# Kernel tuning notes

Hardware: AMD Instinct MI355X
Metric: run time of the kernel (lower is better)

The kernel has to match this reference:

```python
import jax, jax.numpy as jnp
import numpy as np

N_NODES = 100000
N_EDGES = 1600000
NODE_F = 64
EDGE_F = 16
OUT_F = 64


def setup_inputs() -> dict:
    key = jax.random.key(0)
    k1, k2, k3, k4, k5 = jax.random.split(key, 5)
    feat = jax.random.normal(k1, (N_NODES, NODE_F), dtype=jnp.float32)
    edge_feats = jax.random.normal(k2, (N_EDGES, EDGE_F), dtype=jnp.float32)
    src = jax.random.randint(k3, (N_EDGES,), 0, N_NODES, dtype=jnp.int64)
    dst = jax.random.randint(k4, (N_EDGES,), 0, N_NODES, dtype=jnp.int64)
    # xavier-normal-ish weight, zero bias (matches reset_parameters)
    fan_in, fan_out = NODE_F + EDGE_F, OUT_F
    std = (2.0 / (fan_in + fan_out)) ** 0.5
    weight = jax.random.normal(k5, (fan_in, fan_out), dtype=jnp.float32) * std
    bias = jnp.zeros((OUT_F,), dtype=jnp.float32)
    return {"feat": feat, "edge_feats": edge_feats, "src": src, "dst": dst,
            "weight": weight, "bias": bias}


def reference(feat, edge_feats, src, dst, weight, bias):
    N = feat.shape[0]
    # in-degree based symmetric-ish norm: pow(clamp(in_deg,1), -0.5)
    deg = jax.ops.segment_sum(jnp.ones(dst.shape, dtype=feat.dtype), dst,
                              num_segments=N)
    norm = jnp.clip(deg, 1.0) ** -0.5  # [N]
    norm = norm[:, None]
    # sum over incoming edges of concat([edge_feats, h_src]).
    # sum of concat == concat of sums, so aggregate each part separately
    # (avoids materializing the per-edge concat).
    sum_e = jax.ops.segment_sum(edge_feats, dst, num_segments=N)  # [N, E_F]
    sum_h = jax.ops.segment_sum(feat[src], dst, num_segments=N)   # [N, NODE_F]
    sum_f = jnp.concatenate([sum_e, sum_h], axis=-1)              # [N, E_F+NODE_F]
    out = (sum_f * norm) @ weight
    out = out * norm + bias
    return jax.nn.selu(out)
```

## Files before the change

kernel.cpp:

```cpp
#include <hip/hip_runtime.h>
#include <math.h>

#define N_NODES 100000
#define N_EDGES 1600000
#define OUT_F   64
#define NCHUNK  98

#define EQ4      (N_EDGES / 4)
#define CNT_BLK  ((EQ4 + 255) / 256)
#define GEMM_BLK 512
#define K_E      18

typedef __attribute__((ext_vector_type(8))) short bf16x8;
typedef __attribute__((ext_vector_type(4))) float f32x4;

__device__ __forceinline__ unsigned short f2bf_rne(float f) {
    unsigned u = __float_as_uint(f);
    return (unsigned short)((u + 0x7fffu + ((u >> 16) & 1u)) >> 16);
}
__device__ __forceinline__ float bf2f(unsigned short h) {
    return __uint_as_float((unsigned)h << 16);
}

__global__ __launch_bounds__(256) void count_gemm(
    const int* __restrict__ dst, unsigned* __restrict__ pcnt,
    const float* __restrict__ feat, const float* __restrict__ weight,
    unsigned short* __restrict__ G)
{
    __shared__ unsigned lbin[NCHUNK];
    int tid = threadIdx.x;

    if (blockIdx.x < CNT_BLK) {
        if (tid < NCHUNK) lbin[tid] = 0u;
        __syncthreads();
        int q = blockIdx.x * 256 + tid;
        if (q < EQ4) {
            int4 d = ((const int4*)dst)[q];
            atomicAdd(&lbin[d.x >> 10], 1u);
            atomicAdd(&lbin[d.y >> 10], 1u);
            atomicAdd(&lbin[d.z >> 10], 1u);
            atomicAdd(&lbin[d.w >> 10], 1u);
        }
        __syncthreads();
        if (tid < NCHUNK)
            pcnt[(size_t)blockIdx.x * NCHUNK + tid] = lbin[tid];
        return;
    }

    int gb = (int)blockIdx.x - CNT_BLK;
    int wv = tid >> 6, ln = tid & 63;
    int li = ln & 15, lk = ln >> 4;

    bf16x8 Whi[4][2], Wlo[4][2];
    #pragma unroll
    for (int it = 0; it < 4; ++it)
        #pragma unroll
        for (int kb = 0; kb < 2; ++kb)
            #pragma unroll
            for (int j = 0; j < 8; ++j) {
                float w = weight[(16 + kb * 32 + lk * 8 + j) * 64 + it * 16 + li];
                unsigned short h = f2bf_rne(w);
                Whi[it][kb][j] = (short)h;
                Wlo[it][kb][j] = (short)f2bf_rne(w - bf2f(h));
            }

    const int tiles = N_NODES / 16;
    for (int tile = gb * 4 + wv; tile < tiles; tile += GEMM_BLK * 4) {
        int n = tile * 16 + li;
        const float* fr = feat + (size_t)n * 64 + lk * 8;

        bf16x8 Bhi[2], Blo[2];
        #pragma unroll
        for (int kb = 0; kb < 2; ++kb) {
            float4 v0 = *(const float4*)(fr + kb * 32);
            float4 v1 = *(const float4*)(fr + kb * 32 + 4);
            float vv[8] = {v0.x, v0.y, v0.z, v0.w, v1.x, v1.y, v1.z, v1.w};
            #pragma unroll
            for (int j = 0; j < 8; ++j) {
                unsigned short h = f2bf_rne(vv[j]);
                Bhi[kb][j] = (short)h;
                Blo[kb][j] = (short)f2bf_rne(vv[j] - bf2f(h));
            }
        }

        f32x4 acc[4] = {{0.f,0.f,0.f,0.f},{0.f,0.f,0.f,0.f},
                        {0.f,0.f,0.f,0.f},{0.f,0.f,0.f,0.f}};
        #pragma unroll
        for (int kb = 0; kb < 2; ++kb)
            #pragma unroll
            for (int it = 0; it < 4; ++it) {
                acc[it] = __builtin_amdgcn_mfma_f32_16x16x32_bf16(Whi[it][kb], Bhi[kb], acc[it], 0, 0, 0);
                acc[it] = __builtin_amdgcn_mfma_f32_16x16x32_bf16(Wlo[it][kb], Bhi[kb], acc[it], 0, 0, 0);
                acc[it] = __builtin_amdgcn_mfma_f32_16x16x32_bf16(Whi[it][kb], Blo[kb], acc[it], 0, 0, 0);
            }

        #pragma unroll
        for (int it = 0; it < 4; ++it) {
            ushort4 o;
            o.x = f2bf_rne(acc[it][0]);
            o.y = f2bf_rne(acc[it][1]);
            o.z = f2bf_rne(acc[it][2]);
            o.w = f2bf_rne(acc[it][3]);
            *(ushort4*)(G + (size_t)n * 64 + it * 16 + lk * 4) = o;
        }
    }
}

__global__ __launch_bounds__(1024) void colscan(
    const unsigned* __restrict__ pcnt, unsigned* __restrict__ pbase,
    unsigned* __restrict__ ctot)
{
    __shared__ unsigned ws[16];
    int c = blockIdx.x, t = threadIdx.x;
    unsigned j0 = 2u * (unsigned)t, j1 = j0 + 1u;
    unsigned v0 = (j0 < CNT_BLK) ? pcnt[(size_t)j0 * NCHUNK + c] : 0u;
    unsigned v1 = (j1 < CNT_BLK) ? pcnt[(size_t)j1 * NCHUNK + c] : 0u;
    unsigned s = v0 + v1;
    unsigned x = s;
    #pragma unroll
    for (int o = 1; o < 64; o <<= 1) {
        unsigned u = __shfl_up(x, o);
        if ((t & 63) >= o) x += u;
    }
    if ((t & 63) == 63) ws[t >> 6] = x;
    __syncthreads();
    if (t < 16) {
        unsigned y = ws[t];
        #pragma unroll
        for (int o = 1; o < 16; o <<= 1) {
            unsigned u = __shfl_up(y, o);
            if (t >= o) y += u;
        }
        ws[t] = y;
    }
    __syncthreads();
    unsigned excl = ((t >> 6) ? ws[(t >> 6) - 1] : 0u) + x - s;
    if (j0 < CNT_BLK) pbase[(size_t)j0 * NCHUNK + c] = excl;
    if (j1 < CNT_BLK) pbase[(size_t)j1 * NCHUNK + c] = excl + v0;
    if (t == 1023) ctot[c] = excl + s;
}

__global__ __launch_bounds__(128) void scan98(
    const unsigned* __restrict__ ctot, unsigned* __restrict__ cbase)
{
    __shared__ unsigned w0;
    int t = threadIdx.x;
    unsigned v = (t < NCHUNK) ? ctot[t] : 0u;
    unsigned x = v;
    #pragma unroll
    for (int o = 1; o < 64; o <<= 1) {
        unsigned u = __shfl_up(x, o);
        if ((t & 63) >= o) x += u;
    }
    if (t == 63) w0 = x;
    __syncthreads();
    unsigned base = (t >= 64) ? w0 : 0u;
    if (t < NCHUNK) cbase[t] = base + x - v;
}

__global__ __launch_bounds__(256) void scatter(
    const int* __restrict__ src, const int* __restrict__ dst,
    const unsigned* __restrict__ pbase, const unsigned* __restrict__ cbase,
    unsigned long long* __restrict__ csr_pack)
{
    __shared__ unsigned cnt[NCHUNK];
    __shared__ unsigned gb[NCHUNK];
    int tid = threadIdx.x;

    if (tid < NCHUNK) cnt[tid] = 0u;
    __syncthreads();

    int q = blockIdx.x * 256 + tid;
    bool act = q < EQ4;
    int4 d = {0,0,0,0}, s = {0,0,0,0};
    unsigned r0 = 0, r1 = 0, r2 = 0, r3 = 0;
    if (act) {
        d = ((const int4*)dst)[q];
        s = ((const int4*)src)[q];
        r0 = atomicAdd(&cnt[d.x >> 10], 1u);
        r1 = atomicAdd(&cnt[d.y >> 10], 1u);
        r2 = atomicAdd(&cnt[d.z >> 10], 1u);
        r3 = atomicAdd(&cnt[d.w >> 10], 1u);
    }
    if (tid < NCHUNK)
        gb[tid] = cbase[tid] + pbase[(size_t)blockIdx.x * NCHUNK + tid];
    __syncthreads();
    if (act) {
        unsigned e = (unsigned)q * 4u;
        csr_pack[gb[d.x >> 10] + r0] =
            (unsigned long long)((unsigned)s.x | (((unsigned)d.x & 1023u) << 20))
            | ((unsigned long long)(e + 0u) << 32);
        csr_pack[gb[d.y >> 10] + r1] =
            (unsigned long long)((unsigned)s.y | (((unsigned)d.y & 1023u) << 20))
            | ((unsigned long long)(e + 1u) << 32);
        csr_pack[gb[d.z >> 10] + r2] =
            (unsigned long long)((unsigned)s.z | (((unsigned)d.z & 1023u) << 20))
            | ((unsigned long long)(e + 2u) << 32);
        csr_pack[gb[d.w >> 10] + r3] =
            (unsigned long long)((unsigned)s.w | (((unsigned)d.w & 1023u) << 20))
            | ((unsigned long long)(e + 3u) << 32);
    }
}

__global__ __launch_bounds__(1024) void chunk_build(
    const unsigned* __restrict__ ctot, const unsigned* __restrict__ cbase,
    unsigned* __restrict__ off, unsigned long long* __restrict__ csr_pack)
{
    __shared__ unsigned cnt[1024];
    __shared__ unsigned ws[16];
    int t = threadIdx.x, c = blockIdx.x;

    unsigned base = cbase[c];
    unsigned ne   = ctot[c];
    cnt[t] = 0u;
    __syncthreads();

    unsigned long long ev[K_E];
    unsigned rk[K_E];
    #pragma unroll
    for (int k = 0; k < K_E; ++k) {
        unsigned i = (unsigned)t + (unsigned)k * 1024u;
        if (i < ne) {
            ev[k] = csr_pack[base + i];
            rk[k] = atomicAdd(&cnt[(unsigned)(ev[k] >> 20) & 1023u], 1u);
        }
    }
    __syncthreads();

    unsigned v = cnt[t];
    unsigned x = v;
    #pragma unroll
    for (int o = 1; o < 64; o <<= 1) {
        unsigned u = __shfl_up(x, o);
        if ((t & 63) >= o) x += u;
    }
    if ((t & 63) == 63) ws[t >> 6] = x;
    __syncthreads();
    if (t < 16) {
        unsigned y = ws[t];
        #pragma unroll
        for (int o = 1; o < 16; o <<= 1) {
            unsigned u = __shfl_up(y, o);
            if (t >= o) y += u;
        }
        ws[t] = y;
    }
    __syncthreads();
    unsigned excl = ((t >> 6) ? ws[(t >> 6) - 1] : 0u) + x - v;

    int gnode = c * 1024 + t;
    if (gnode < N_NODES) off[gnode] = base + excl;
    if (c == NCHUNK - 1 && t == 0) off[N_NODES] = N_EDGES;

    __syncthreads();
    cnt[t] = base + excl;
    __syncthreads();

    #pragma unroll
    for (int k = 0; k < K_E; ++k) {
        unsigned i = (unsigned)t + (unsigned)k * 1024u;
        if (i < ne) {
            unsigned dl = (unsigned)(ev[k] >> 20) & 1023u;
            csr_pack[cnt[dl] + rk[k]] = ev[k] & 0xFFFFFFFF000FFFFFull;
        }
    }
}

__global__ __launch_bounds__(256) void gather_out(
    const unsigned short* __restrict__ G,
    const float* __restrict__ edge_feats,
    const unsigned long long* __restrict__ csr_pack,
    const unsigned* __restrict__ off,
    const float* __restrict__ weight,
    const float* __restrict__ bias,
    float* __restrict__ out)
{
    int tid = threadIdx.x;
    int wv = tid >> 6, ln = tid & 63;

    float We[16];
    #pragma unroll
    for (int k = 0; k < 16; ++k) We[k] = weight[k * 64 + ln];
    float b = bias[ln];

    const float SC = 1.0507009873554805f;
    const float AL = 1.6732632423543772f;

    int n = blockIdx.x * 4 + wv;
    if (n >= N_NODES) return;

    unsigned start = off[n], end = off[n + 1];
    float norm2 = __builtin_amdgcn_rcpf(fmaxf((float)(end - start), 1.0f));

    const int gq = ln >> 4;
    const int eq = ln >> 2;

    float gh4[4] = {0.f, 0.f, 0.f, 0.f};
    float ae4[4] = {0.f, 0.f, 0.f, 0.f};

    const ushort4* __restrict__ Gv = (const ushort4*)G;

    for (unsigned base = start; base < end; base += 64u) {
        unsigned m = min(64u, end - base);
        unsigned lo = 0u, hi = 0u;
        if ((unsigned)ln < m) {
            unsigned long long pk = csr_pack[base + (unsigned)ln];
            lo = (unsigned)pk;
            hi = (unsigned)(pk >> 32);
        }

        for (unsigned i = 0; i < m; i += 8u) {
            unsigned i0 = i + (unsigned)gq, i1 = i0 + 4u;
            unsigned s0 = __shfl(lo, (int)min(i0, m - 1u));
            unsigned s1 = __shfl(lo, (int)min(i1, m - 1u));
            ushort4 q0 = {0,0,0,0}, q1 = {0,0,0,0};
            if (i0 < m) q0 = Gv[(size_t)s0 * 16u + (unsigned)(ln & 15)];
            if (i1 < m) q1 = Gv[(size_t)s1 * 16u + (unsigned)(ln & 15)];
            gh4[0] += __uint_as_float((unsigned)q0.x << 16) + __uint_as_float((unsigned)q1.x << 16);
            gh4[1] += __uint_as_float((unsigned)q0.y << 16) + __uint_as_float((unsigned)q1.y << 16);
            gh4[2] += __uint_as_float((unsigned)q0.z << 16) + __uint_as_float((unsigned)q1.z << 16);
            gh4[3] += __uint_as_float((unsigned)q0.w << 16) + __uint_as_float((unsigned)q1.w << 16);
        }

        for (unsigned i = 0; i < m; i += 16u) {
            unsigned ie = i + (unsigned)eq;
            unsigned e0 = __shfl(hi, (int)min(ie, m - 1u));
            if (ie < m) {
                float4 v = *(const float4*)(edge_feats + (size_t)e0 * 16u + (unsigned)(ln & 3) * 4u);
                ae4[0] += v.x; ae4[1] += v.y; ae4[2] += v.z; ae4[3] += v.w;
            }
        }
    }

    #pragma unroll
    for (int c = 0; c < 4; ++c) {
        gh4[c] += __shfl_xor(gh4[c], 16);
        gh4[c] += __shfl_xor(gh4[c], 32);
        ae4[c] += __shfl_xor(ae4[c], 4);
        ae4[c] += __shfl_xor(ae4[c], 8);
        ae4[c] += __shfl_xor(ae4[c], 16);
        ae4[c] += __shfl_xor(ae4[c], 32);
    }
    int srcl = ln >> 2;
    float r0 = __shfl(gh4[0], srcl);
    float r1 = __shfl(gh4[1], srcl);
    float r2 = __shfl(gh4[2], srcl);
    float r3 = __shfl(gh4[3], srcl);
    int c = ln & 3;
    float gh = (c & 2) ? ((c & 1) ? r3 : r2) : ((c & 1) ? r1 : r0);

    float acc = gh;
    #pragma unroll
    for (int k = 0; k < 16; ++k)
        acc = fmaf(__shfl(ae4[k & 3], k >> 2), We[k], acc);

    float o = acc * norm2 + b;
    out[(size_t)n * 64u + ln] = (o > 0.f) ? SC * o : SC * AL * (__expf(o) - 1.0f);
}

extern "C" void kernel_launch(void* const* d_in, const int* in_sizes, int n_in,
                              void* d_out, int out_size, void* d_ws, size_t ws_size,
                              hipStream_t stream) {
    const float* feat       = (const float*)d_in[0];
    const float* edge_feats = (const float*)d_in[1];
    const int*   src        = (const int*)d_in[2];
    const int*   dst        = (const int*)d_in[3];
    const float* weight     = (const float*)d_in[4];
    const float* bias       = (const float*)d_in[5];
    float* out = (float*)d_out;

    unsigned long long* csr_pack = (unsigned long long*)d_ws;
    unsigned short* G = (unsigned short*)(csr_pack + N_EDGES);
    unsigned* off   = (unsigned*)(G + (size_t)N_NODES * 64);
    unsigned* pcnt  = off + N_NODES + 1;
    unsigned* pbase = pcnt + (size_t)CNT_BLK * NCHUNK;
    unsigned* ctot  = pbase + (size_t)CNT_BLK * NCHUNK;
    unsigned* cbase = ctot + NCHUNK;

    count_gemm<<<dim3(CNT_BLK + GEMM_BLK), dim3(256), 0, stream>>>(
        dst, pcnt, feat, weight, G);
    colscan<<<dim3(NCHUNK), dim3(1024), 0, stream>>>(pcnt, pbase, ctot);
    scan98<<<dim3(1), dim3(128), 0, stream>>>(ctot, cbase);
    scatter<<<dim3(CNT_BLK), dim3(256), 0, stream>>>(
        src, dst, pbase, cbase, csr_pack);
    chunk_build<<<dim3(NCHUNK), dim3(1024), 0, stream>>>(
        ctot, cbase, off, csr_pack);
    gather_out<<<dim3((N_NODES + 3) / 4), dim3(256), 0, stream>>>(
        G, edge_feats, csr_pack, off, weight, bias, out);
}
```

Baseline: 297.6 us.

## Fuse scan kernels, stage scatter in LDS, process two nodes per wave

The single-block chunk-total scan is folded into the column-scan kernel using a last-block-done atomic counter, which removes one launch. The scatter kernel now sorts each block's packed edges by chunk in LDS before writing, so global stores land in more contiguous runs. The gather kernel has each wave handle two destination nodes with interleaved loops, giving more independent memory loads in flight. The costs are a threadfence and atomic per block, extra LDS traffic in scatter, and more registers in gather.

```diff
diff --git a/kernel.cpp b/kernel.cpp
--- a/kernel.cpp
+++ b/kernel.cpp
@@ -25,7 +25,7 @@
 __global__ __launch_bounds__(256) void count_gemm(
     const int* __restrict__ dst, unsigned* __restrict__ pcnt,
     const float* __restrict__ feat, const float* __restrict__ weight,
-    unsigned short* __restrict__ G)
+    unsigned short* __restrict__ G, unsigned* __restrict__ done)
 {
     __shared__ unsigned lbin[NCHUNK];
     int tid = threadIdx.x;
@@ -48,6 +48,8 @@
     }
 
     int gb = (int)blockIdx.x - CNT_BLK;
+    if (gb == 0 && tid == 0) *done = 0u;
+
     int wv = tid >> 6, ln = tid & 63;
     int li = ln & 15, lk = ln >> 4;
 
@@ -106,11 +108,13 @@
     }
 }
 
-__global__ __launch_bounds__(1024) void colscan(
+__global__ __launch_bounds__(1024) void colscan_cbase(
     const unsigned* __restrict__ pcnt, unsigned* __restrict__ pbase,
-    unsigned* __restrict__ ctot)
+    unsigned* __restrict__ ctot, unsigned* __restrict__ cbase,
+    unsigned* __restrict__ done)
 {
     __shared__ unsigned ws[16];
+    __shared__ unsigned isLast;
     int c = blockIdx.x, t = threadIdx.x;
     unsigned j0 = 2u * (unsigned)t, j1 = j0 + 1u;
     unsigned v0 = (j0 < CNT_BLK) ? pcnt[(size_t)j0 * NCHUNK + c] : 0u;
@@ -138,24 +142,24 @@
     if (j0 < CNT_BLK) pbase[(size_t)j0 * NCHUNK + c] = excl;
     if (j1 < CNT_BLK) pbase[(size_t)j1 * NCHUNK + c] = excl + v0;
     if (t == 1023) ctot[c] = excl + s;
-}
-
-__global__ __launch_bounds__(128) void scan98(
-    const unsigned* __restrict__ ctot, unsigned* __restrict__ cbase)
-{
-    __shared__ unsigned w0;
-    int t = threadIdx.x;
-    unsigned v = (t < NCHUNK) ? ctot[t] : 0u;
-    unsigned x = v;
+
+    __threadfence();
+    if (t == 0) isLast = (atomicAdd(done, 1u) == NCHUNK - 1u) ? 1u : 0u;
+    __syncthreads();
+    if (!isLast) return;
+
+    int ln = t & 63, wv = t >> 6;
+    unsigned v = (t < NCHUNK) ? atomicAdd(&ctot[t], 0u) : 0u;
+    unsigned y = v;
     #pragma unroll
     for (int o = 1; o < 64; o <<= 1) {
-        unsigned u = __shfl_up(x, o);
-        if ((t & 63) >= o) x += u;
-    }
-    if (t == 63) w0 = x;
-    __syncthreads();
-    unsigned base = (t >= 64) ? w0 : 0u;
-    if (t < NCHUNK) cbase[t] = base + x - v;
+        unsigned u = __shfl_up(y, o);
+        if (ln >= o) y += u;
+    }
+    if (ln == 63) ws[wv] = y;
+    __syncthreads();
+    unsigned base = (wv == 1) ? ws[0] : 0u;
+    if (t < NCHUNK) cbase[t] = base + y - v;
 }
 
 __global__ __launch_bounds__(256) void scatter(
@@ -164,8 +168,12 @@
     unsigned long long* __restrict__ csr_pack)
 {
     __shared__ unsigned cnt[NCHUNK];
-    __shared__ unsigned gb[NCHUNK];
-    int tid = threadIdx.x;
+    __shared__ unsigned gbs[NCHUNK];
+    __shared__ unsigned lbase[NCHUNK];
+    __shared__ unsigned wsum[4];
+    __shared__ unsigned long long sval[1024];
+    __shared__ unsigned sadr[1024];
+    int tid = threadIdx.x, wv = tid >> 6, ln = tid & 63;
 
     if (tid < NCHUNK) cnt[tid] = 0u;
     __syncthreads();
@@ -183,23 +191,46 @@
         r3 = atomicAdd(&cnt[d.w >> 10], 1u);
     }
     if (tid < NCHUNK)
-        gb[tid] = cbase[tid] + pbase[(size_t)blockIdx.x * NCHUNK + tid];
-    __syncthreads();
+        gbs[tid] = cbase[tid] + pbase[(size_t)blockIdx.x * NCHUNK + tid];
+    __syncthreads();
+
+    unsigned v = (tid < NCHUNK) ? cnt[tid] : 0u;
+    unsigned x = v;
+    #pragma unroll
+    for (int o = 1; o < 64; o <<= 1) {
+        unsigned u = __shfl_up(x, o);
+        if (ln >= o) x += u;
+    }
+    if (ln == 63) wsum[wv] = x;
+    __syncthreads();
+    unsigned excl = x - v + ((wv == 1) ? wsum[0] : 0u);
+    unsigned tot = wsum[0] + wsum[1];
+    if (tid < NCHUNK) lbase[tid] = excl;
+    __syncthreads();
+
     if (act) {
         unsigned e = (unsigned)q * 4u;
-        csr_pack[gb[d.x >> 10] + r0] =
-            (unsigned long long)((unsigned)s.x | (((unsigned)d.x & 1023u) << 20))
-            | ((unsigned long long)(e + 0u) << 32);
-        csr_pack[gb[d.y >> 10] + r1] =
-            (unsigned long long)((unsigned)s.y | (((unsigned)d.y & 1023u) << 20))
-            | ((unsigned long long)(e + 1u) << 32);
-        csr_pack[gb[d.z >> 10] + r2] =
-            (unsigned long long)((unsigned)s.z | (((unsigned)d.z & 1023u) << 20))
-            | ((unsigned long long)(e + 2u) << 32);
-        csr_pack[gb[d.w >> 10] + r3] =
-            (unsigned long long)((unsigned)s.w | (((unsigned)d.w & 1023u) << 20))
-            | ((unsigned long long)(e + 3u) << 32);
-    }
+        unsigned c0 = (unsigned)d.x >> 10, c1 = (unsigned)d.y >> 10;
+        unsigned c2 = (unsigned)d.z >> 10, c3 = (unsigned)d.w >> 10;
+        unsigned p0 = lbase[c0] + r0, p1 = lbase[c1] + r1;
+        unsigned p2 = lbase[c2] + r2, p3 = lbase[c3] + r3;
+        sval[p0] = (unsigned long long)((unsigned)s.x | (((unsigned)d.x & 1023u) << 20))
+                 | ((unsigned long long)(e + 0u) << 32);
+        sadr[p0] = gbs[c0] + r0;
+        sval[p1] = (unsigned long long)((unsigned)s.y | (((unsigned)d.y & 1023u) << 20))
+                 | ((unsigned long long)(e + 1u) << 32);
+        sadr[p1] = gbs[c1] + r1;
+        sval[p2] = (unsigned long long)((unsigned)s.z | (((unsigned)d.z & 1023u) << 20))
+                 | ((unsigned long long)(e + 2u) << 32);
+        sadr[p2] = gbs[c2] + r2;
+        sval[p3] = (unsigned long long)((unsigned)s.w | (((unsigned)d.w & 1023u) << 20))
+                 | ((unsigned long long)(e + 3u) << 32);
+        sadr[p3] = gbs[c3] + r3;
+    }
+    __syncthreads();
+
+    for (unsigned i = tid; i < tot; i += 256u)
+        csr_pack[sadr[i]] = sval[i];
 }
 
 __global__ __launch_bounds__(1024) void chunk_build(
@@ -264,6 +295,31 @@
             csr_pack[cnt[dl] + rk[k]] = ev[k] & 0xFFFFFFFF000FFFFFull;
         }
     }
+}
+
+__device__ __forceinline__ float node_finish(
+    float gh4[4], float ae4[4], int ln, const float* We)
+{
+    #pragma unroll
+    for (int c = 0; c < 4; ++c) {
+        gh4[c] += __shfl_xor(gh4[c], 16);
+        gh4[c] += __shfl_xor(gh4[c], 32);
+        ae4[c] += __shfl_xor(ae4[c], 4);
+        ae4[c] += __shfl_xor(ae4[c], 8);
+        ae4[c] += __shfl_xor(ae4[c], 16);
+        ae4[c] += __shfl_xor(ae4[c], 32);
+    }
+    int srcl = ln >> 2;
+    float r0 = __shfl(gh4[0], srcl);
+    float r1 = __shfl(gh4[1], srcl);
+    float r2 = __shfl(gh4[2], srcl);
+    float r3 = __shfl(gh4[3], srcl);
+    int c = ln & 3;
+    float acc = (c & 2) ? ((c & 1) ? r3 : r2) : ((c & 1) ? r1 : r0);
+    #pragma unroll
+    for (int k = 0; k < 16; ++k)
+        acc = fmaf(__shfl(ae4[k & 3], k >> 2), We[k], acc);
+    return acc;
 }
 
 __global__ __launch_bounds__(256) void gather_out(
@@ -278,84 +334,97 @@
     int tid = threadIdx.x;
     int wv = tid >> 6, ln = tid & 63;
 
+    const float SC = 1.0507009873554805f;
+    const float AL = 1.6732632423543772f;
+
+    const int gq = ln >> 4;
+    const int eq = ln >> 2;
+    const ushort4* __restrict__ Gv = (const ushort4*)G;
+
+    int nA = blockIdx.x * 8 + wv * 2;
+    unsigned o0 = off[nA], o1 = off[nA + 1], o2 = off[nA + 2];
+
+    float ghA[4] = {0.f,0.f,0.f,0.f}, aeA[4] = {0.f,0.f,0.f,0.f};
+    float ghB[4] = {0.f,0.f,0.f,0.f}, aeB[4] = {0.f,0.f,0.f,0.f};
+
+    unsigned baseA = o0, baseB = o1;
+    while (baseA < o1 || baseB < o2) {
+        unsigned mA = (baseA < o1) ? min(64u, o1 - baseA) : 0u;
+        unsigned mB = (baseB < o2) ? min(64u, o2 - baseB) : 0u;
+        unsigned loA = 0u, hiA = 0u, loB = 0u, hiB = 0u;
+        if ((unsigned)ln < mA) {
+            unsigned long long pk = csr_pack[baseA + (unsigned)ln];
+            loA = (unsigned)pk; hiA = (unsigned)(pk >> 32);
+        }
+        if ((unsigned)ln < mB) {
+            unsigned long long pk = csr_pack[baseB + (unsigned)ln];
+            loB = (unsigned)pk; hiB = (unsigned)(pk >> 32);
+        }
+        unsigned mm = mA > mB ? mA : mB;
+
+        for (unsigned i = 0; i < mm; i += 8u) {
+            if (i < mA) {
+                unsigned i0 = i + (unsigned)gq, i1 = i0 + 4u;
+                unsigned s0 = __shfl(loA, (int)min(i0, mA - 1u));
+                unsigned s1 = __shfl(loA, (int)min(i1, mA - 1u));
+                ushort4 q0 = {0,0,0,0}, q1 = {0,0,0,0};
+                if (i0 < mA) q0 = Gv[(size_t)s0 * 16u + (unsigned)(ln & 15)];
+                if (i1 < mA) q1 = Gv[(size_t)s1 * 16u + (unsigned)(ln & 15)];
+                ghA[0] += __uint_as_float((unsigned)q0.x << 16) + __uint_as_float((unsigned)q1.x << 16);
+                ghA[1] += __uint_as_float((unsigned)q0.y << 16) + __uint_as_float((unsigned)q1.y << 16);
+                ghA[2] += __uint_as_float((unsigned)q0.z << 16) + __uint_as_float((unsigned)q1.z << 16);
+                ghA[3] += __uint_as_float((unsigned)q0.w << 16) + __uint_as_float((unsigned)q1.w << 16);
+            }
+            if (i < mB) {
+                unsigned i0 = i + (unsigned)gq, i1 = i0 + 4u;
+                unsigned s0 = __shfl(loB, (int)min(i0, mB - 1u));
+                unsigned s1 = __shfl(loB, (int)min(i1, mB - 1u));
+                ushort4 q0 = {0,0,0,0}, q1 = {0,0,0,0};
+                if (i0 < mB) q0 = Gv[(size_t)s0 * 16u + (unsigned)(ln & 15)];
+                if (i1 < mB) q1 = Gv[(size_t)s1 * 16u + (unsigned)(ln & 15)];
+                ghB[0] += __uint_as_float((unsigned)q0.x << 16) + __uint_as_float((unsigned)q1.x << 16);
+                ghB[1] += __uint_as_float((unsigned)q0.y << 16) + __uint_as_float((unsigned)q1.y << 16);
+                ghB[2] += __uint_as_float((unsigned)q0.z << 16) + __uint_as_float((unsigned)q1.z << 16);
+                ghB[3] += __uint_as_float((unsigned)q0.w << 16) + __uint_as_float((unsigned)q1.w << 16);
+            }
+        }
+
+        for (unsigned i = 0; i < mm; i += 16u) {
+            if (i < mA) {
+                unsigned ie = i + (unsigned)eq;
+                unsigned e0 = __shfl(hiA, (int)min(ie, mA - 1u));
+                if (ie < mA) {
+                    float4 v = *(const float4*)(edge_feats + (size_t)e0 * 16u + (unsigned)(ln & 3) * 4u);
+                    aeA[0] += v.x; aeA[1] += v.y; aeA[2] += v.z; aeA[3] += v.w;
+                }
+            }
+            if (i < mB) {
+                unsigned ie = i + (unsigned)eq;
+                unsigned e0 = __shfl(hiB, (int)min(ie, mB - 1u));
+                if (ie < mB) {
+                    float4 v = *(const float4*)(edge_feats + (size_t)e0 * 16u + (unsigned)(ln & 3) * 4u);
+                    aeB[0] += v.x; aeB[1] += v.y; aeB[2] += v.z; aeB[3] += v.w;
+                }
+            }
+        }
+        baseA += 64u; baseB += 64u;
+    }
+
     float We[16];
     #pragma unroll
     for (int k = 0; k < 16; ++k) We[k] = weight[k * 64 + ln];
     float b = bias[ln];
 
-    const float SC = 1.0507009873554805f;
-    const float AL = 1.6732632423543772f;
-
-    int n = blockIdx.x * 4 + wv;
-    if (n >= N_NODES) return;
-
-    unsigned start = off[n], end = off[n + 1];
-    float norm2 = __builtin_amdgcn_rcpf(fmaxf((float)(end - start), 1.0f));
-
-    const int gq = ln >> 4;
-    const int eq = ln >> 2;
-
-    float gh4[4] = {0.f, 0.f, 0.f, 0.f};
-    float ae4[4] = {0.f, 0.f, 0.f, 0.f};
-
-    const ushort4* __restrict__ Gv = (const ushort4*)G;
-
-    for (unsigned base = start; base < end; base += 64u) {
-        unsigned m = min(64u, end - base);
-        unsigned lo = 0u, hi = 0u;
-        if ((unsigned)ln < m) {
-            unsigned long long pk = csr_pack[base + (unsigned)ln];
-            lo = (unsigned)pk;
-            hi = (unsigned)(pk >> 32);
-        }
-
-        for (unsigned i = 0; i < m; i += 8u) {
-            unsigned i0 = i + (unsigned)gq, i1 = i0 + 4u;
-            unsigned s0 = __shfl(lo, (int)min(i0, m - 1u));
-            unsigned s1 = __shfl(lo, (int)min(i1, m - 1u));
-            ushort4 q0 = {0,0,0,0}, q1 = {0,0,0,0};
-            if (i0 < m) q0 = Gv[(size_t)s0 * 16u + (unsigned)(ln & 15)];
-            if (i1 < m) q1 = Gv[(size_t)s1 * 16u + (unsigned)(ln & 15)];
-            gh4[0] += __uint_as_float((unsigned)q0.x << 16) + __uint_as_float((unsigned)q1.x << 16);
-            gh4[1] += __uint_as_float((unsigned)q0.y << 16) + __uint_as_float((unsigned)q1.y << 16);
-            gh4[2] += __uint_as_float((unsigned)q0.z << 16) + __uint_as_float((unsigned)q1.z << 16);
-            gh4[3] += __uint_as_float((unsigned)q0.w << 16) + __uint_as_float((unsigned)q1.w << 16);
-        }
-
-        for (unsigned i = 0; i < m; i += 16u) {
-            unsigned ie = i + (unsigned)eq;
-            unsigned e0 = __shfl(hi, (int)min(ie, m - 1u));
-            if (ie < m) {
-                float4 v = *(const float4*)(edge_feats + (size_t)e0 * 16u + (unsigned)(ln & 3) * 4u);
-                ae4[0] += v.x; ae4[1] += v.y; ae4[2] += v.z; ae4[3] += v.w;
-            }
-        }
-    }
-
-    #pragma unroll
-    for (int c = 0; c < 4; ++c) {
-        gh4[c] += __shfl_xor(gh4[c], 16);
-        gh4[c] += __shfl_xor(gh4[c], 32);
-        ae4[c] += __shfl_xor(ae4[c], 4);
-        ae4[c] += __shfl_xor(ae4[c], 8);
-        ae4[c] += __shfl_xor(ae4[c], 16);
-        ae4[c] += __shfl_xor(ae4[c], 32);
-    }
-    int srcl = ln >> 2;
-    float r0 = __shfl(gh4[0], srcl);
-    float r1 = __shfl(gh4[1], srcl);
-    float r2 = __shfl(gh4[2], srcl);
-    float r3 = __shfl(gh4[3], srcl);
-    int c = ln & 3;
-    float gh = (c & 2) ? ((c & 1) ? r3 : r2) : ((c & 1) ? r1 : r0);
-
-    float acc = gh;
-    #pragma unroll
-    for (int k = 0; k < 16; ++k)
-        acc = fmaf(__shfl(ae4[k & 3], k >> 2), We[k], acc);
-
-    float o = acc * norm2 + b;
-    out[(size_t)n * 64u + ln] = (o > 0.f) ? SC * o : SC * AL * (__expf(o) - 1.0f);
+    float normA = __builtin_amdgcn_rcpf(fmaxf((float)(o1 - o0), 1.0f));
+    float normB = __builtin_amdgcn_rcpf(fmaxf((float)(o2 - o1), 1.0f));
+
+    float accA = node_finish(ghA, aeA, ln, We);
+    float accB = node_finish(ghB, aeB, ln, We);
+
+    float oA = accA * normA + b;
+    float oB = accB * normB + b;
+    out[(size_t)nA * 64u + ln]       = (oA > 0.f) ? SC * oA : SC * AL * (__expf(oA) - 1.0f);
+    out[(size_t)(nA + 1) * 64u + ln] = (oB > 0.f) ? SC * oB : SC * AL * (__expf(oB) - 1.0f);
 }
 
 extern "C" void kernel_launch(void* const* d_in, const int* in_sizes, int n_in,
@@ -376,15 +445,16 @@
     unsigned* pbase = pcnt + (size_t)CNT_BLK * NCHUNK;
     unsigned* ctot  = pbase + (size_t)CNT_BLK * NCHUNK;
     unsigned* cbase = ctot + NCHUNK;
+    unsigned* done  = cbase + NCHUNK;
 
     count_gemm<<<dim3(CNT_BLK + GEMM_BLK), dim3(256), 0, stream>>>(
-        dst, pcnt, feat, weight, G);
-    colscan<<<dim3(NCHUNK), dim3(1024), 0, stream>>>(pcnt, pbase, ctot);
-    scan98<<<dim3(1), dim3(128), 0, stream>>>(ctot, cbase);
+        dst, pcnt, feat, weight, G, done);
+    colscan_cbase<<<dim3(NCHUNK), dim3(1024), 0, stream>>>(
+        pcnt, pbase, ctot, cbase, done);
     scatter<<<dim3(CNT_BLK), dim3(256), 0, stream>>>(
         src, dst, pbase, cbase, csr_pack);
     chunk_build<<<dim3(NCHUNK), dim3(1024), 0, stream>>>(
         ctot, cbase, off, csr_pack);
-    gather_out<<<dim3((N_NODES + 3) / 4), dim3(256), 0, stream>>>(
+    gather_out<<<dim3(N_NODES / 8), dim3(256), 0, stream>>>(
         G, edge_feats, csr_pack, off, weight, bias, out);
 }
```

Result: slower. 329.1 us (+10.6%).
